# Performance work log

Hardware: AMD Instinct MI355X
Metric: run time of the kernel (lower is better)

The kernel has to match this reference:

```python
import jax, jax.numpy as jnp
import numpy as np

BATCH, SEQ, D_MODEL = 2, 4096, 1024
D_STATE, EXPAND = 64, 2
D_INNER = D_MODEL * EXPAND


def setup_inputs() -> dict:
    key = jax.random.key(0)
    ks = jax.random.split(key, 12)
    s = 0.02
    return {
        "x": jax.random.normal(ks[0], (BATCH, SEQ, D_MODEL), dtype=jnp.float32),
        "W_in": jax.random.normal(ks[1], (D_MODEL, 2 * D_INNER), dtype=jnp.float32) * s,
        "b_in": jnp.zeros((2 * D_INNER,), dtype=jnp.float32),
        "W_xp": jax.random.normal(ks[2], (D_INNER, D_STATE), dtype=jnp.float32) * s,
        "b_xp": jnp.zeros((D_STATE,), dtype=jnp.float32),
        "W_dt": jax.random.normal(ks[3], (D_INNER, D_MODEL), dtype=jnp.float32) * s,
        "b_dt": jnp.zeros((D_MODEL,), dtype=jnp.float32),
        "W_out": jax.random.normal(ks[4], (D_INNER, D_MODEL), dtype=jnp.float32) * s,
        "b_out": jnp.zeros((D_MODEL,), dtype=jnp.float32),
        "A_log": jax.random.normal(ks[5], (D_STATE,), dtype=jnp.float32),
        "D": jax.random.normal(ks[6], (D_MODEL,), dtype=jnp.float32),
    }


def _silu(v):
    return v * jax.nn.sigmoid(v)


def reference(x, W_in, b_in, W_xp, b_xp, W_dt, b_dt, W_out, b_out, A_log, D):
    # in_proj -> split into inner stream and residual gate
    xr = x @ W_in + b_in                       # [B,S,2*d_inner]
    x_inner, res = jnp.split(xr, 2, axis=-1)   # each [B,S,d_inner]
    x_inner = _silu(x_inner)

    A = -jnp.exp(A_log)                        # [N]
    delta = jax.nn.softplus(x_inner @ W_dt + b_dt)  # [B,S,d_model]
    mean_delta = delta.mean(axis=-1)           # [B,S] (scalar dt per step, as in source)
    a = jnp.exp(A[None, None, :] * mean_delta[..., None])  # [B,S,N] discrete A
    bx = x_inner @ W_xp + b_xp                 # [B,S,N] input injection

    # sequential selective-scan recurrence: state = a_t * state + bx_t
    def step(state, inp):
        a_t, bx_t = inp                        # [B,N] each
        state = a_t * state + bx_t
        return state, state.sum(axis=-1)       # emit per-batch scalar

    init = jnp.zeros((x.shape[0], D_STATE), dtype=x.dtype)
    _, s_sum = jax.lax.scan(step, init, (a.transpose(1, 0, 2), bx.transpose(1, 0, 2)))
    s_sum = s_sum.T                            # [B,S]

    y = s_sum[..., None] * x_inner             # [B,S,d_inner]
    y = y * _silu(res)
    out = y @ W_out + b_out + x * D
    return out
```

## Files before the change

### kernel.cpp

```cpp
#include <hip/hip_runtime.h>

#define SEQ 4096
#define DMODEL 1024
#define DSTATE 64
#define DINNER 2048
#define MROWS 8192
#define NCAT 1152
#define NCHUNK 64
#define LCHUNK 64

typedef __attribute__((ext_vector_type(8))) __bf16 bf16x8;
typedef __attribute__((ext_vector_type(8))) short short8;
typedef __attribute__((ext_vector_type(4))) float floatx4;

__device__ inline float bf2f(short s) {
  union { unsigned u; float f; } c;
  c.u = ((unsigned)(unsigned short)s) << 16;
  return c.f;
}
__device__ inline short f2bf(float f) {
  union { float f; unsigned u; } c; c.f = f;
  unsigned r = 0x7fffu + ((c.u >> 16) & 1u);
  return (short)((c.u + r) >> 16);
}
__device__ inline float silu_f(float v) {
  return v * __builtin_amdgcn_rcpf(1.f + __expf(-v));
}
__device__ inline float softplus_f(float v) {
  return fmaxf(v, 0.f) + log1pf(__expf(-fabsf(v)));
}
__device__ inline void gld_lds16(const void* g, void* l) {
  __builtin_amdgcn_global_load_lds(
      (__attribute__((address_space(1))) void*)g,
      (__attribute__((address_space(3))) void*)l, 16, 0, 0);
}

__device__ inline size_t permOff(int r, int k, int K) {
  return (((size_t)(r >> 4) * (K >> 3) + (k >> 3)) << 7) + ((r & 15) << 3) + (k & 7);
}

#define PP0 4096
#define PP1 (PP0 + 4096)
#define PP2 (PP1 + 2048)
#define PP3 (PP2 + 128)
#define PP4 (PP3 + 2048)

__device__ void tile_transpose_perm(const float* __restrict__ in, short* __restrict__ out,
                                    int R, int C, int bx, int by, float (*tile)[33]) {
  const int tx = threadIdx.x & 31, ty = threadIdx.x >> 5;
  const int cb = bx * 32, rb = by * 32;
#pragma unroll
  for (int i = 0; i < 32; i += 8) {
    int r = rb + ty + i, c = cb + tx;
    tile[ty + i][tx] = (r < R && c < C) ? in[(size_t)r * C + c] : 0.f;
  }
  __syncthreads();
#pragma unroll
  for (int i = 0; i < 32; i += 8) {
    int orow = cb + ty + i, oc = rb + tx;
    if (orow < C && oc < R) out[permOff(orow, oc, R)] = f2bf(tile[tx][ty + i]);
  }
}

__global__ void prepass_kernel(const float* __restrict__ x, short* __restrict__ x_bf,
                               const float* __restrict__ W_in, short* __restrict__ Wt_in,
                               const float* __restrict__ W_dt, const float* __restrict__ W_xp,
                               short* __restrict__ Bcat,
                               const float* __restrict__ W_out, short* __restrict__ Wt_out) {
  __shared__ float tile[32][33];
  const int blk = blockIdx.x;
  if (blk < PP0) {
    int o = blk * 256 + threadIdx.x;
    int m = o & 15, rest = o >> 4;
    int c = rest & 127, p = rest >> 7;
    const float* src = x + ((size_t)(p * 16 + m)) * 1024 + c * 8;
    float4 v0 = ((const float4*)src)[0];
    float4 v1 = ((const float4*)src)[1];
    short8 ov;
    ov[0] = f2bf(v0.x); ov[1] = f2bf(v0.y); ov[2] = f2bf(v0.z); ov[3] = f2bf(v0.w);
    ov[4] = f2bf(v1.x); ov[5] = f2bf(v1.y); ov[6] = f2bf(v1.z); ov[7] = f2bf(v1.w);
    ((short8*)x_bf)[o] = ov;
  } else if (blk < PP1) {
    int t = blk - PP0;
    tile_transpose_perm(W_in, Wt_in, 1024, 4096, t & 127, t >> 7, tile);
  } else if (blk < PP2) {
    int t = blk - PP1;
    tile_transpose_perm(W_dt, Bcat, 2048, 1024, t & 31, t >> 5, tile);
  } else if (blk < PP3) {
    int t = blk - PP2;
    tile_transpose_perm(W_xp, Bcat + (size_t)1024 * DINNER, 2048, 64, t & 1, t >> 1, tile);
  } else {
    int t = blk - PP3;
    tile_transpose_perm(W_out, Wt_out, 2048, 1024, t & 31, t >> 5, tile);
  }
}

template <int MODE>
__global__ __launch_bounds__(256) void gemm_bt(
    const short* __restrict__ A, const short* __restrict__ Bt,
    const float* __restrict__ bias,
    void* __restrict__ out0, void* __restrict__ out1,
    int M, int N, int K, int KSL)
{
  __shared__ __attribute__((aligned(16))) short sA[128 * 32];
  __shared__ __attribute__((aligned(16))) short sB[128 * 32];

  const int tid = threadIdx.x;
  const int lane = tid & 63;
  const int w = tid >> 6;
  const int wr = w >> 1, wc = w & 1;
  const int m = lane & 15, quad = lane >> 4;
  const int bM = blockIdx.y * 128, bN = blockIdx.x * 128;

  floatx4 acc[4][4] = {};

  const size_t PS = (size_t)K * 16;
  const short* Apan0 = A  + ((size_t)(bM >> 4) + w) * PS + lane * 8;
  const short* Apan1 = Apan0 + 4 * PS;
  const short* Bpan0 = Bt + ((size_t)(bN >> 4) + w) * PS + lane * 8;
  const short* Bpan1 = Bpan0 + 4 * PS;
  short* dA0 = sA + w * 512;
  short* dA1 = sA + (w + 4) * 512;
  short* dB0 = sB + w * 512;
  short* dB1 = sB + (w + 4) * 512;

  const int kbeg = blockIdx.z * KSL;
  for (int k0 = kbeg; k0 < kbeg + KSL; k0 += 32) {
    __syncthreads();
    const size_t ko = (size_t)k0 * 16;
    gld_lds16(Apan0 + ko, dA0);
    gld_lds16(Apan1 + ko, dA1);
    gld_lds16(Bpan0 + ko, dB0);
    gld_lds16(Bpan1 + ko, dB1);
    __syncthreads();
    bf16x8 af[4], bf[4];
#pragma unroll
    for (int rt = 0; rt < 4; ++rt)
      af[rt] = *(const bf16x8*)(sA + (((wr * 4 + rt) * 64 + quad * 16 + m) << 3));
#pragma unroll
    for (int ct = 0; ct < 4; ++ct)
      bf[ct] = *(const bf16x8*)(sB + (((wc * 4 + ct) * 64 + quad * 16 + m) << 3));
#pragma unroll
    for (int rt = 0; rt < 4; ++rt)
#pragma unroll
      for (int ct = 0; ct < 4; ++ct)
        acc[rt][ct] = __builtin_amdgcn_mfma_f32_16x16x32_bf16(af[rt], bf[ct], acc[rt][ct], 0, 0, 0);
  }

  const int rowbase = bM + wr * 64;
  const int colbase = bN + wc * 64;

  if (MODE == 0) {
    short* dst = (bN < DINNER) ? (short*)out0 : (short*)out1;
    const int cb = (bN < DINNER) ? colbase : colbase - DINNER;
#pragma unroll
    for (int rt = 0; rt < 4; ++rt) {
      const size_t rowPan = ((size_t)((rowbase >> 4) + rt)) << 8;
#pragma unroll
      for (int ct = 0; ct < 4; ++ct) {
        const int colA = colbase + ct * 16 + m;
        const int colP = cb + ct * 16 + m;
        const size_t base = ((rowPan + (colP >> 3)) << 7) + (colP & 7) + ((size_t)quad * 32);
#pragma unroll
        for (int reg = 0; reg < 4; ++reg) {
          float val = acc[rt][ct][reg] + bias[colA];
          dst[base + reg * 8] = f2bf(silu_f(val));
        }
      }
    }
  } else {
    short* dst = (short*)out0 + (size_t)blockIdx.z * M * N;
#pragma unroll
    for (int rt = 0; rt < 4; ++rt)
#pragma unroll
      for (int ct = 0; ct < 4; ++ct) {
        const int col = colbase + ct * 16 + m;
#pragma unroll
        for (int reg = 0; reg < 4; ++reg) {
          const int r = rowbase + rt * 16 + quad * 4 + reg;
          dst[(size_t)r * N + col] = f2bf(acc[rt][ct][reg]);
        }
      }
  }
}

__global__ void g2_epilogue(const short* __restrict__ p, const float* __restrict__ b_dt,
                            const float* __restrict__ b_xp,
                            float* __restrict__ md_sum, float* __restrict__ bx) {
  const int r = blockIdx.x, t = threadIdx.x;
  const size_t base0 = (size_t)r * NCAT;
  const size_t base1 = base0 + (size_t)MROWS * NCAT;
  float s = 0.f;
#pragma unroll
  for (int j = 0; j < 4; ++j) {
    const int c = t + j * 256;
    float v = bf2f(p[base0 + c]) + bf2f(p[base1 + c]) + b_dt[c];
    s += softplus_f(v);
  }
  s += __shfl_xor(s, 1);  s += __shfl_xor(s, 2);  s += __shfl_xor(s, 4);
  s += __shfl_xor(s, 8);  s += __shfl_xor(s, 16); s += __shfl_xor(s, 32);
  __shared__ float wsum[4];
  if ((t & 63) == 0) wsum[t >> 6] = s;
  __syncthreads();
  if (t == 0) md_sum[r] = wsum[0] + wsum[1] + wsum[2] + wsum[3];
  if (t < 64)
    bx[(size_t)r * DSTATE + t] =
        bf2f(p[base0 + 1024 + t]) + bf2f(p[base1 + 1024 + t]) + b_xp[t];
}

__global__ void g4_epilogue(const short* __restrict__ p, const float* __restrict__ b_out,
                            const float* __restrict__ x, const float* __restrict__ Dv,
                            float* __restrict__ out) {
  const int r = blockIdx.x, c = threadIdx.x * 4;
  const size_t o = (size_t)r * DMODEL + c;
  short4 a0 = *(const short4*)(p + o);
  short4 a1 = *(const short4*)(p + (size_t)MROWS * DMODEL + o);
  float4 xv = *(const float4*)(x + o);
  float4 ov;
  ov.x = bf2f(a0.x) + bf2f(a1.x) + b_out[c + 0] + xv.x * Dv[c + 0];
  ov.y = bf2f(a0.y) + bf2f(a1.y) + b_out[c + 1] + xv.y * Dv[c + 1];
  ov.z = bf2f(a0.z) + bf2f(a1.z) + b_out[c + 2] + xv.z * Dv[c + 2];
  ov.w = bf2f(a0.w) + bf2f(a1.w) + b_out[c + 3] + xv.w * Dv[c + 3];
  *(float4*)(out + o) = ov;
}

__global__ void scan_phase1(const float* __restrict__ md_sum, const float* __restrict__ A_log,
                            const float* __restrict__ bx, float* __restrict__ a_buf,
                            float* __restrict__ chunk_prod, float* __restrict__ chunk_end) {
  const int n = threadIdx.x;
  const int c = blockIdx.x & (NCHUNK - 1);
  const int b = blockIdx.x >> 6;
  const float An = -__expf(A_log[n]);
  float prod = 1.f, st = 0.f;
  const int t0 = c * LCHUNK;
  for (int i = 0; i < LCHUNK; ++i) {
    const int t = t0 + i;
    const float md = md_sum[b * SEQ + t] * (1.f / DMODEL);
    const float a = __expf(An * md);
    const size_t idx = ((size_t)(b * SEQ + t)) * DSTATE + n;
    st = a * st + bx[idx];
    prod *= a;
    a_buf[idx] = a;
  }
  chunk_prod[(b * NCHUNK + c) * DSTATE + n] = prod;
  chunk_end [(b * NCHUNK + c) * DSTATE + n] = st;
}

__global__ void scan_phase2(const float* __restrict__ chunk_prod,
                            const float* __restrict__ chunk_end,
                            float* __restrict__ chunk_init) {
  const int i = threadIdx.x;
  const int b = i >> 6, n = i & 63;
  float st = 0.f;
  for (int c = 0; c < NCHUNK; ++c) {
    const size_t idx = ((size_t)(b * NCHUNK + c)) * DSTATE + n;
    chunk_init[idx] = st;
    st = chunk_prod[idx] * st + chunk_end[idx];
  }
}

__global__ void scan_phase3(const float* __restrict__ a_buf, const float* __restrict__ bx,
                            const float* __restrict__ chunk_init, float* __restrict__ s_sum) {
  const int n = threadIdx.x;
  const int c = blockIdx.x & (NCHUNK - 1);
  const int b = blockIdx.x >> 6;
  float st = chunk_init[((size_t)(b * NCHUNK + c)) * DSTATE + n];
  const int t0 = c * LCHUNK;
  for (int i = 0; i < LCHUNK; ++i) {
    const int t = t0 + i;
    const size_t idx = ((size_t)(b * SEQ + t)) * DSTATE + n;
    st = a_buf[idx] * st + bx[idx];
    float v = st;
    v += __shfl_xor(v, 32); v += __shfl_xor(v, 16); v += __shfl_xor(v, 8);
    v += __shfl_xor(v, 4);  v += __shfl_xor(v, 2);  v += __shfl_xor(v, 1);
    if (n == 0) s_sum[b * SEQ + t] = v;
  }
}

__global__ void ymul_kernel(const short* __restrict__ xi, const short* __restrict__ g,
                            const float* __restrict__ s_sum, short* __restrict__ y) {
  const int o = blockIdx.x * 256 + threadIdx.x;
  const int row = ((o >> 12) << 4) | (o & 15);
  const size_t base = (size_t)o * 8;
  const float s = s_sum[row];
  short8 xv = *(const short8*)(xi + base);
  short8 gv = *(const short8*)(g + base);
  short8 yv;
#pragma unroll
  for (int k = 0; k < 8; ++k) yv[k] = f2bf(s * bf2f(xv[k]) * bf2f(gv[k]));
  *(short8*)(y + base) = yv;
}

extern "C" void kernel_launch(void* const* d_in, const int* in_sizes, int n_in,
                              void* d_out, int out_size, void* d_ws, size_t ws_size,
                              hipStream_t stream) {
  const float* x     = (const float*)d_in[0];
  const float* W_in  = (const float*)d_in[1];
  const float* b_in  = (const float*)d_in[2];
  const float* W_xp  = (const float*)d_in[3];
  const float* b_xp  = (const float*)d_in[4];
  const float* W_dt  = (const float*)d_in[5];
  const float* b_dt  = (const float*)d_in[6];
  const float* W_out = (const float*)d_in[7];
  const float* b_out = (const float*)d_in[8];
  const float* A_log = (const float*)d_in[9];
  const float* Dv    = (const float*)d_in[10];

  char* ws = (char*)d_ws;
  size_t off = 0;
  auto alloc = [&](size_t bytes) -> void* {
    void* p = (void*)(ws + off);
    off += (bytes + 255) & ~(size_t)255;
    return p;
  };
  short* x_bf    = (short*)alloc((size_t)MROWS * DMODEL * 2);
  short* Wt_in   = (short*)alloc((size_t)4096 * 1024 * 2);
  short* Bcat    = (short*)alloc((size_t)NCAT * DINNER * 2);
  short* Wt_out  = (short*)alloc((size_t)1024 * 2048 * 2);
  short* xi      = (short*)alloc((size_t)MROWS * DINNER * 2);
  short* gbuf    = (short*)alloc((size_t)MROWS * DINNER * 2);
  short* ybuf    = (short*)alloc((size_t)MROWS * DINNER * 2);
  short* p2      = (short*)alloc((size_t)2 * MROWS * NCAT * 2);
  float* md_sum  = (float*)alloc((size_t)MROWS * 4);
  float* bx      = (float*)alloc((size_t)MROWS * DSTATE * 4);
  float* a_buf   = (float*)alloc((size_t)MROWS * DSTATE * 4);
  float* cprod   = (float*)alloc((size_t)2 * NCHUNK * DSTATE * 4);
  float* cend    = (float*)alloc((size_t)2 * NCHUNK * DSTATE * 4);
  float* cinit   = (float*)alloc((size_t)2 * NCHUNK * DSTATE * 4);
  float* s_sum   = (float*)alloc((size_t)MROWS * 4);

  prepass_kernel<<<PP4, 256, 0, stream>>>(x, x_bf, W_in, Wt_in, W_dt, W_xp, Bcat, W_out, Wt_out);

  gemm_bt<0><<<dim3(4096 / 128, MROWS / 128, 1), 256, 0, stream>>>(
      x_bf, Wt_in, b_in, xi, gbuf, MROWS, 4096, 1024, 1024);
  gemm_bt<1><<<dim3(NCAT / 128, MROWS / 128, 2), 256, 0, stream>>>(
      xi, Bcat, nullptr, p2, nullptr, MROWS, NCAT, 2048, 1024);
  g2_epilogue<<<MROWS, 256, 0, stream>>>(p2, b_dt, b_xp, md_sum, bx);
  scan_phase1<<<2 * NCHUNK, DSTATE, 0, stream>>>(md_sum, A_log, bx, a_buf, cprod, cend);
  scan_phase2<<<1, 128, 0, stream>>>(cprod, cend, cinit);
  scan_phase3<<<2 * NCHUNK, DSTATE, 0, stream>>>(a_buf, bx, cinit, s_sum);
  ymul_kernel<<<MROWS * DINNER / 8 / 256, 256, 0, stream>>>(xi, gbuf, s_sum, ybuf);
  gemm_bt<1><<<dim3(1024 / 128, MROWS / 128, 2), 256, 0, stream>>>(
      ybuf, Wt_out, nullptr, xi, nullptr, MROWS, 1024, 2048, 1024);
  g4_epilogue<<<MROWS, 256, 0, stream>>>(xi, b_out, x, Dv, (float*)d_out);
}
```

Before: 435.9 us.

## Swizzle GEMM blocks across XCDs, template shapes, and fuse scan phases

```diff
diff --git a/kernel.cpp b/kernel.cpp
--- a/kernel.cpp
+++ b/kernel.cpp
@@ -95,12 +95,11 @@
   }
 }
 
-template <int MODE>
+template <int MODE, int KTOT, int KSL, int NB, int Z>
 __global__ __launch_bounds__(256) void gemm_bt(
     const short* __restrict__ A, const short* __restrict__ Bt,
     const float* __restrict__ bias,
-    void* __restrict__ out0, void* __restrict__ out1,
-    int M, int N, int K, int KSL)
+    void* __restrict__ out0, void* __restrict__ out1)
 {
   __shared__ __attribute__((aligned(16))) short sA[128 * 32];
   __shared__ __attribute__((aligned(16))) short sB[128 * 32];
@@ -110,11 +109,19 @@
   const int w = tid >> 6;
   const int wr = w >> 1, wc = w & 1;
   const int m = lane & 15, quad = lane >> 4;
-  const int bM = blockIdx.y * 128, bN = blockIdx.x * 128;
+
+  const int xcd = blockIdx.x & 7;
+  const int rest = blockIdx.x >> 3;
+  constexpr int PXB = 8 * NB;
+  const int z = rest / PXB;
+  const int q2 = rest - z * PXB;
+  const int bM = (xcd * 8 + (q2 & 7)) * 128;
+  const int bN = (q2 >> 3) * 128;
+  constexpr int N = NB * 128;
 
   floatx4 acc[4][4] = {};
 
-  const size_t PS = (size_t)K * 16;
+  const size_t PS = (size_t)KTOT * 16;
   const short* Apan0 = A  + ((size_t)(bM >> 4) + w) * PS + lane * 8;
   const short* Apan1 = Apan0 + 4 * PS;
   const short* Bpan0 = Bt + ((size_t)(bN >> 4) + w) * PS + lane * 8;
@@ -124,7 +131,8 @@
   short* dB0 = sB + w * 512;
   short* dB1 = sB + (w + 4) * 512;
 
-  const int kbeg = blockIdx.z * KSL;
+  const int kbeg = z * KSL;
+#pragma unroll 2
   for (int k0 = kbeg; k0 < kbeg + KSL; k0 += 32) {
     __syncthreads();
     const size_t ko = (size_t)k0 * 16;
@@ -169,7 +177,7 @@
       }
     }
   } else {
-    short* dst = (short*)out0 + (size_t)blockIdx.z * M * N;
+    short* dst = (short*)out0 + (size_t)z * MROWS * N;
 #pragma unroll
     for (int rt = 0; rt < 4; ++rt)
 #pragma unroll
@@ -225,7 +233,7 @@
 }
 
 __global__ void scan_phase1(const float* __restrict__ md_sum, const float* __restrict__ A_log,
-                            const float* __restrict__ bx, float* __restrict__ a_buf,
+                            const float* __restrict__ bx,
                             float* __restrict__ chunk_prod, float* __restrict__ chunk_end) {
   const int n = threadIdx.x;
   const int c = blockIdx.x & (NCHUNK - 1);
@@ -237,39 +245,33 @@
     const int t = t0 + i;
     const float md = md_sum[b * SEQ + t] * (1.f / DMODEL);
     const float a = __expf(An * md);
-    const size_t idx = ((size_t)(b * SEQ + t)) * DSTATE + n;
-    st = a * st + bx[idx];
+    st = a * st + bx[((size_t)(b * SEQ + t)) * DSTATE + n];
     prod *= a;
-    a_buf[idx] = a;
   }
   chunk_prod[(b * NCHUNK + c) * DSTATE + n] = prod;
   chunk_end [(b * NCHUNK + c) * DSTATE + n] = st;
 }
 
-__global__ void scan_phase2(const float* __restrict__ chunk_prod,
+__global__ void scan_phase3(const float* __restrict__ md_sum, const float* __restrict__ A_log,
+                            const float* __restrict__ bx,
+                            const float* __restrict__ chunk_prod,
                             const float* __restrict__ chunk_end,
-                            float* __restrict__ chunk_init) {
-  const int i = threadIdx.x;
-  const int b = i >> 6, n = i & 63;
-  float st = 0.f;
-  for (int c = 0; c < NCHUNK; ++c) {
-    const size_t idx = ((size_t)(b * NCHUNK + c)) * DSTATE + n;
-    chunk_init[idx] = st;
-    st = chunk_prod[idx] * st + chunk_end[idx];
-  }
-}
-
-__global__ void scan_phase3(const float* __restrict__ a_buf, const float* __restrict__ bx,
-                            const float* __restrict__ chunk_init, float* __restrict__ s_sum) {
+                            float* __restrict__ s_sum) {
   const int n = threadIdx.x;
   const int c = blockIdx.x & (NCHUNK - 1);
   const int b = blockIdx.x >> 6;
-  float st = chunk_init[((size_t)(b * NCHUNK + c)) * DSTATE + n];
+  const float An = -__expf(A_log[n]);
+  float st = 0.f;
+  for (int cc = 0; cc < c; ++cc) {
+    const size_t idx = ((size_t)(b * NCHUNK + cc)) * DSTATE + n;
+    st = chunk_prod[idx] * st + chunk_end[idx];
+  }
   const int t0 = c * LCHUNK;
   for (int i = 0; i < LCHUNK; ++i) {
     const int t = t0 + i;
-    const size_t idx = ((size_t)(b * SEQ + t)) * DSTATE + n;
-    st = a_buf[idx] * st + bx[idx];
+    const float md = md_sum[b * SEQ + t] * (1.f / DMODEL);
+    const float a = __expf(An * md);
+    st = a * st + bx[((size_t)(b * SEQ + t)) * DSTATE + n];
     float v = st;
     v += __shfl_xor(v, 32); v += __shfl_xor(v, 16); v += __shfl_xor(v, 8);
     v += __shfl_xor(v, 4);  v += __shfl_xor(v, 2);  v += __shfl_xor(v, 1);
@@ -323,24 +325,18 @@
   short* p2      = (short*)alloc((size_t)2 * MROWS * NCAT * 2);
   float* md_sum  = (float*)alloc((size_t)MROWS * 4);
   float* bx      = (float*)alloc((size_t)MROWS * DSTATE * 4);
-  float* a_buf   = (float*)alloc((size_t)MROWS * DSTATE * 4);
   float* cprod   = (float*)alloc((size_t)2 * NCHUNK * DSTATE * 4);
   float* cend    = (float*)alloc((size_t)2 * NCHUNK * DSTATE * 4);
-  float* cinit   = (float*)alloc((size_t)2 * NCHUNK * DSTATE * 4);
   float* s_sum   = (float*)alloc((size_t)MROWS * 4);
 
   prepass_kernel<<<PP4, 256, 0, stream>>>(x, x_bf, W_in, Wt_in, W_dt, W_xp, Bcat, W_out, Wt_out);
 
-  gemm_bt<0><<<dim3(4096 / 128, MROWS / 128, 1), 256, 0, stream>>>(
-      x_bf, Wt_in, b_in, xi, gbuf, MROWS, 4096, 1024, 1024);
-  gemm_bt<1><<<dim3(NCAT / 128, MROWS / 128, 2), 256, 0, stream>>>(
-      xi, Bcat, nullptr, p2, nullptr, MROWS, NCAT, 2048, 1024);
+  gemm_bt<0, 1024, 1024, 32, 1><<<2048, 256, 0, stream>>>(x_bf, Wt_in, b_in, xi, gbuf);
+  gemm_bt<1, 2048, 1024, 9, 2><<<1152, 256, 0, stream>>>(xi, Bcat, nullptr, p2, nullptr);
   g2_epilogue<<<MROWS, 256, 0, stream>>>(p2, b_dt, b_xp, md_sum, bx);
-  scan_phase1<<<2 * NCHUNK, DSTATE, 0, stream>>>(md_sum, A_log, bx, a_buf, cprod, cend);
-  scan_phase2<<<1, 128, 0, stream>>>(cprod, cend, cinit);
-  scan_phase3<<<2 * NCHUNK, DSTATE, 0, stream>>>(a_buf, bx, cinit, s_sum);
+  scan_phase1<<<2 * NCHUNK, DSTATE, 0, stream>>>(md_sum, A_log, bx, cprod, cend);
+  scan_phase3<<<2 * NCHUNK, DSTATE, 0, stream>>>(md_sum, A_log, bx, cprod, cend, s_sum);
   ymul_kernel<<<MROWS * DINNER / 8 / 256, 256, 0, stream>>>(xi, gbuf, s_sum, ybuf);
-  gemm_bt<1><<<dim3(1024 / 128, MROWS / 128, 2), 256, 0, stream>>>(
-      ybuf, Wt_out, nullptr, xi, nullptr, MROWS, 1024, 2048, 1024);
+  gemm_bt<1, 2048, 1024, 8, 2><<<1024, 256, 0, stream>>>(ybuf, Wt_out, nullptr, xi, nullptr);
   g4_epilogue<<<MROWS, 256, 0, stream>>>(xi, b_out, x, Dv, (float*)d_out);
 }
```

New measurement: 418.3 us. -4.0%, faster.
